# Performance work log

Hardware: AMD Instinct MI355X
Metric: run time of the kernel (lower is better)

## Reference

```python
import jax, jax.numpy as jnp
import numpy as np

B, N_IN, NODE, L = 4, 128, 32, 256
N_HID, N_OUT = 64, 128
D_IN = N_HID          # d_inner = expand(1) * d_model
D_STATE = 2 * N_HID   # d_state = n_hid * 2
D_CONV = 2
DT_RANK = max(1, -(-N_HID // 16))  # ceil(d_model/16) = 4


def setup_inputs() -> dict:
    key = jax.random.key(0)
    ks = jax.random.split(key, 12)
    s = lambda k, shape, scale: (jax.random.normal(k, shape, jnp.float32) * scale)
    inputs = jax.random.normal(ks[0], (B, N_IN, NODE, L), jnp.float32)
    return {
        "inputs": inputs,
        "w_in": s(ks[1], (N_HID, N_IN), 1.0 / np.sqrt(N_IN)),
        "b_in": jnp.zeros((N_HID,), jnp.float32),
        "in_proj_w": s(ks[2], (2 * D_IN, N_HID), 1.0 / np.sqrt(N_HID)),
        "conv_w": s(ks[3], (D_IN, D_CONV), 0.5),
        "conv_b": jnp.zeros((D_IN,), jnp.float32),
        "x_proj_w": s(ks[4], (DT_RANK + 2 * D_STATE, D_IN), 1.0 / np.sqrt(D_IN)),
        "dt_proj_w": s(ks[5], (D_IN, DT_RANK), DT_RANK ** -0.5),
        "dt_proj_b": s(ks[6], (D_IN,), 0.1),
        "A_log": jnp.log(jnp.tile(jnp.arange(1, D_STATE + 1, dtype=jnp.float32)[None, :], (D_IN, 1))),
        "D": jnp.ones((D_IN,), jnp.float32),
        "out_proj_w": s(ks[7], (N_HID, D_IN), 1.0 / np.sqrt(D_IN)),
        "w_out": s(ks[8], (N_OUT, N_HID), 1.0 / np.sqrt(N_HID)),
        "b_out": jnp.zeros((N_OUT,), jnp.float32),
        "ln_w": jnp.ones((L, N_OUT), jnp.float32),
        "ln_b": jnp.zeros((L, N_OUT), jnp.float32),
    }


def _mamba(x, in_proj_w, conv_w, conv_b, x_proj_w, dt_proj_w, dt_proj_b, A_log, D, out_proj_w):
    # x: (Bseq, L, d_model)
    Bs, Ls, _ = x.shape
    d_state = A_log.shape[1]
    dt_rank = dt_proj_w.shape[1]
    d_conv = conv_w.shape[1]

    xz = x @ in_proj_w.T                     # (Bs, L, 2*d_inner)
    xm, z = jnp.split(xz, 2, axis=-1)

    # causal depthwise conv1d (padding = d_conv-1, truncated to L)
    xp = jnp.pad(xm, ((0, 0), (d_conv - 1, 0), (0, 0)))
    xc = sum(xp[:, k:k + Ls, :] * conv_w[:, k] for k in range(d_conv)) + conv_b
    xc = jax.nn.silu(xc)                     # (Bs, L, d_inner)

    dbc = xc @ x_proj_w.T                    # (Bs, L, dt_rank + 2*d_state)
    dt = dbc[..., :dt_rank]
    Bm = dbc[..., dt_rank:dt_rank + d_state]
    Cm = dbc[..., dt_rank + d_state:]
    delta = jax.nn.softplus(dt @ dt_proj_w.T + dt_proj_b)  # (Bs, L, d_inner)
    A = -jnp.exp(A_log)                      # (d_inner, d_state)

    def step(h, inp):
        dlt, Bt, Ct, xt = inp                # (Bs,d), (Bs,s), (Bs,s), (Bs,d)
        dA = jnp.exp(dlt[:, :, None] * A)    # (Bs, d, s)
        h = dA * h + (dlt * xt)[:, :, None] * Bt[:, None, :]
        y = jnp.einsum('bds,bs->bd', h, Ct)
        return h, y

    h0 = jnp.zeros((Bs, xm.shape[-1], d_state), x.dtype)
    xs = (delta.transpose(1, 0, 2), Bm.transpose(1, 0, 2),
          Cm.transpose(1, 0, 2), xc.transpose(1, 0, 2))
    _, ys = jax.lax.scan(step, h0, xs)       # ys: (L, Bs, d_inner)

    y = ys.transpose(1, 0, 2) + xc * D
    y = y * jax.nn.silu(z)
    return y @ out_proj_w.T                  # (Bs, L, d_model)


def reference(inputs, w_in, b_in, in_proj_w, conv_w, conv_b, x_proj_w,
              dt_proj_w, dt_proj_b, A_log, D, out_proj_w,
              w_out, b_out, ln_w, ln_b):
    b, n_in, node, seq = inputs.shape
    # permute(0,2,3,1).reshape(B*node, L, n_in)
    x = inputs.transpose(0, 2, 3, 1).reshape(b * node, seq, n_in)
    x = x @ w_in.T + b_in
    x = jax.nn.silu(_mamba(x, in_proj_w, conv_w, conv_b, x_proj_w,
                           dt_proj_w, dt_proj_b, A_log, D, out_proj_w))
    x = x @ w_out.T + b_out                  # (B*node, L, n_out)
    # LayerNorm over last two dims [feature_len, n_out]
    mu = x.mean(axis=(-2, -1), keepdims=True)
    var = ((x - mu) ** 2).mean(axis=(-2, -1), keepdims=True)
    x = (x - mu) / jnp.sqrt(var + 1e-5) * ln_w + ln_b
    return x.reshape(b, node, seq, -1).transpose(0, 3, 1, 2)
```

## Files before the change

### kernel.cpp

```cpp
#include <hip/hip_runtime.h>
#include <math.h>


__device__ __forceinline__ float silu_f(float v) { return v / (1.f + __expf(-v)); }
__device__ __forceinline__ float softplus_f(float v) { return v > 20.f ? v : log1pf(__expf(v)); }

#if __has_builtin(__builtin_amdgcn_exp2f)
#define EXP2N(x) __builtin_amdgcn_exp2f(x)
#else
#define EXP2N(x) __expf((x) * 0.6931471805599453f)
#endif

__global__ __launch_bounds__(256) void k1_proj(
    const float* __restrict__ inp, const float* __restrict__ w_in,
    const float* __restrict__ b_in, const float* __restrict__ ipw,
    float* __restrict__ XM, float* __restrict__ Zb)
{
  __shared__ float sIN[128*64];
  __shared__ float sW[64*68];
  __shared__ float sXT[64*68];
  const int bid = blockIdx.x;
  const int r = bid >> 2, tb = bid & 3;
  const int b = r >> 5, node = r & 31;
  const int t0 = tb * 64;
  const int tid = threadIdx.x;
  const int tg = tid & 15, vg = tid >> 4;
  const int tl0 = tg * 4, v0 = vg * 4;

  for (int e = tid; e < 128*64; e += 256) {
    int i = e >> 6, t = e & 63;
    sIN[e] = inp[((b*128 + i)*32 + node)*256 + t0 + t];
  }

  float acc[4][4];
  #pragma unroll
  for (int ti = 0; ti < 4; ti++)
    #pragma unroll
    for (int j = 0; j < 4; j++) acc[ti][j] = b_in[v0 + j];

  for (int kc = 0; kc < 2; kc++) {
    __syncthreads();
    for (int e = tid; e < 64*16; e += 256) {
      int row = e >> 4, c4 = e & 15;
      *(float4*)&sW[row*68 + c4*4] = *(const float4*)&w_in[row*128 + kc*64 + c4*4];
    }
    __syncthreads();
    for (int k4 = 0; k4 < 16; k4++) {
      float4 wv[4];
      #pragma unroll
      for (int j = 0; j < 4; j++)
        wv[j] = *(const float4*)&sW[(v0 + j)*68 + k4*4];
      #pragma unroll
      for (int kk = 0; kk < 4; kk++) {
        float4 x4 = *(const float4*)&sIN[(kc*64 + k4*4 + kk)*64 + tl0];
        #pragma unroll
        for (int j = 0; j < 4; j++) {
          float w = kk==0 ? wv[j].x : kk==1 ? wv[j].y : kk==2 ? wv[j].z : wv[j].w;
          acc[0][j] = fmaf(x4.x, w, acc[0][j]);
          acc[1][j] = fmaf(x4.y, w, acc[1][j]);
          acc[2][j] = fmaf(x4.z, w, acc[2][j]);
          acc[3][j] = fmaf(x4.w, w, acc[3][j]);
        }
      }
    }
  }
  #pragma unroll
  for (int j = 0; j < 4; j++)
    *(float4*)&sXT[(v0 + j)*68 + tl0] =
        make_float4(acc[0][j], acc[1][j], acc[2][j], acc[3][j]);

  for (int pass = 0; pass < 2; pass++) {
    __syncthreads();
    for (int e = tid; e < 64*16; e += 256) {
      int row = e >> 4, c4 = e & 15;
      *(float4*)&sW[row*68 + c4*4] = *(const float4*)&ipw[(pass*64 + row)*64 + c4*4];
    }
    __syncthreads();

    float a2[4][4];
    #pragma unroll
    for (int ti = 0; ti < 4; ti++)
      #pragma unroll
      for (int j = 0; j < 4; j++) a2[ti][j] = 0.f;

    for (int k4 = 0; k4 < 16; k4++) {
      float4 wv[4];
      #pragma unroll
      for (int j = 0; j < 4; j++)
        wv[j] = *(const float4*)&sW[(v0 + j)*68 + k4*4];
      #pragma unroll
      for (int kk = 0; kk < 4; kk++) {
        float4 x4 = *(const float4*)&sXT[(k4*4 + kk)*68 + tl0];
        #pragma unroll
        for (int j = 0; j < 4; j++) {
          float w = kk==0 ? wv[j].x : kk==1 ? wv[j].y : kk==2 ? wv[j].z : wv[j].w;
          a2[0][j] = fmaf(x4.x, w, a2[0][j]);
          a2[1][j] = fmaf(x4.y, w, a2[1][j]);
          a2[2][j] = fmaf(x4.z, w, a2[2][j]);
          a2[3][j] = fmaf(x4.w, w, a2[3][j]);
        }
      }
    }

    float* dst = (pass == 0) ? XM : Zb;
    #pragma unroll
    for (int ti = 0; ti < 4; ti++)
      *(float4*)&dst[(r*256 + t0 + tl0 + ti)*64 + v0] =
          make_float4(a2[ti][0], a2[ti][1], a2[ti][2], a2[ti][3]);
  }
}

__global__ __launch_bounds__(256) void k2_conv_xproj(
    const float* __restrict__ XM, const float* __restrict__ convw,
    const float* __restrict__ convb, const float* __restrict__ xpw,
    const float* __restrict__ dtw, const float* __restrict__ dtb,
    float* __restrict__ XC, float* __restrict__ DELTA,
    float* __restrict__ BM, float* __restrict__ CM)
{
  __shared__ float sXM[65*64];
  __shared__ float sXC[64*68];
  __shared__ float sW[64*68];
  __shared__ float sDT[64*5];
  const int bid = blockIdx.x;
  const int r = bid >> 2, tb = bid & 3;
  const int t0 = tb * 64;
  const int tid = threadIdx.x;
  const int tg = tid & 15, vg = tid >> 4;
  const int tl0 = tg * 4, v0 = vg * 4;

  for (int e = tid; e < 65*64; e += 256) {
    int tt = e >> 6, d = e & 63;
    int tgl = t0 - 1 + tt;
    sXM[e] = (tgl < 0) ? 0.f : XM[(r*256 + tgl)*64 + d];
  }
  __syncthreads();

  for (int e = tid; e < 64*64; e += 256) {
    int t = e >> 6, d = e & 63;
    float c0 = convw[d*2], c1 = convw[d*2 + 1];
    float pre = fmaf(sXM[t*64 + d], c0, fmaf(sXM[(t+1)*64 + d], c1, convb[d]));
    float v = silu_f(pre);
    sXC[d*68 + t] = v;
    XC[(r*256 + t0 + t)*64 + d] = v;
  }

  for (int pass = 0; pass < 5; pass++) {
    __syncthreads();
    for (int e = tid; e < 64*16; e += 256) {
      int row = e >> 4, c4 = e & 15;
      int grow = pass*64 + row;
      float4 w = (grow < 260) ? *(const float4*)&xpw[grow*64 + c4*4]
                              : make_float4(0.f, 0.f, 0.f, 0.f);
      *(float4*)&sW[row*68 + c4*4] = w;
    }
    __syncthreads();

    float acc[4][4];
    #pragma unroll
    for (int ti = 0; ti < 4; ti++)
      #pragma unroll
      for (int jj = 0; jj < 4; jj++) acc[ti][jj] = 0.f;

    for (int k4 = 0; k4 < 16; k4++) {
      float4 wv[4];
      #pragma unroll
      for (int jj = 0; jj < 4; jj++)
        wv[jj] = *(const float4*)&sW[(v0 + jj)*68 + k4*4];
      #pragma unroll
      for (int kk = 0; kk < 4; kk++) {
        float4 x4 = *(const float4*)&sXC[(k4*4 + kk)*68 + tl0];
        #pragma unroll
        for (int jj = 0; jj < 4; jj++) {
          float w = kk==0 ? wv[jj].x : kk==1 ? wv[jj].y : kk==2 ? wv[jj].z : wv[jj].w;
          acc[0][jj] = fmaf(x4.x, w, acc[0][jj]);
          acc[1][jj] = fmaf(x4.y, w, acc[1][jj]);
          acc[2][jj] = fmaf(x4.z, w, acc[2][jj]);
          acc[3][jj] = fmaf(x4.w, w, acc[3][jj]);
        }
      }
    }

    const int j0g = pass*64 + v0;
    if (j0g < 4) {
      #pragma unroll
      for (int ti = 0; ti < 4; ti++)
        #pragma unroll
        for (int jj = 0; jj < 4; jj++)
          sDT[(tl0 + ti)*5 + jj] = acc[ti][jj];
    } else if (j0g < 132) {
      #pragma unroll
      for (int ti = 0; ti < 4; ti++)
        *(float4*)&BM[(r*256 + t0 + tl0 + ti)*128 + (j0g - 4)] =
            make_float4(acc[ti][0], acc[ti][1], acc[ti][2], acc[ti][3]);
    } else if (j0g < 260) {
      #pragma unroll
      for (int ti = 0; ti < 4; ti++)
        *(float4*)&CM[(r*256 + t0 + tl0 + ti)*128 + (j0g - 132)] =
            make_float4(acc[ti][0], acc[ti][1], acc[ti][2], acc[ti][3]);
    }
  }
  __syncthreads();

  for (int e = tid; e < 64*64; e += 256) {
    int t = e >> 6, d = e & 63;
    float4 w4 = *(const float4*)&dtw[d*4];
    float x = dtb[d];
    x = fmaf(sDT[t*5 + 0], w4.x, x);
    x = fmaf(sDT[t*5 + 1], w4.y, x);
    x = fmaf(sDT[t*5 + 2], w4.z, x);
    x = fmaf(sDT[t*5 + 3], w4.w, x);
    DELTA[(r*256 + t0 + t)*64 + d] = softplus_f(x);
  }
}

__global__ __launch_bounds__(256) void k3_scan(
    const float* __restrict__ DELTA, const float* __restrict__ XC,
    const float* __restrict__ BM, const float* __restrict__ CM,
    const float* __restrict__ alog, float* __restrict__ YP)
{
  const int bid = blockIdx.x;
  const int r = bid & 127;
  const int rest = bid >> 7;
  const int sc = rest & 1;
  const int dc = rest >> 1;
  const int tid = threadIdx.x;
  const int dg = tid >> 4;
  const int sg = tid & 15;
  const int sl0 = sg * 4;
  const int d = dc*16 + dg;
  const float LOG2E = 1.44269504f;

  float a2[4], h[4];
  #pragma unroll
  for (int j = 0; j < 4; j++) {
    a2[j] = -expf(alog[d*128 + sc*64 + sl0 + j]) * LOG2E;
    h[j] = 0.f;
  }

  const float* pB = BM    + r*256*128 + sc*64 + sl0;
  const float* pC = CM    + r*256*128 + sc*64 + sl0;
  const float* pD = DELTA + r*256*64  + d;
  const float* pX = XC    + r*256*64  + d;
  float*       pY = YP + ((size_t)(sc*128 + r))*256*64 + d;

  float4 vB0, vC0, vB1, vC1, vB2, vC2, vB3, vC3;
  float  vD0, vX0, vD1, vX1, vD2, vX2, vD3, vX3;

#define K3_LD(SET, T_) do { \
    vB##SET = *(const float4*)(pB + (T_)*128); \
    vC##SET = *(const float4*)(pC + (T_)*128); \
    vD##SET = pD[(T_)*64]; \
    vX##SET = pX[(T_)*64]; \
  } while (0)

#define K3_STEP(SET, T_) do { \
    float dl = vD##SET, xv = vX##SET; \
    float4 Bv = vB##SET, Cv = vC##SET; \
    float u = dl * xv; \
    float y; \
    float dA0 = EXP2N(dl * a2[0]); \
    h[0] = fmaf(dA0, h[0], u * Bv.x); \
    y = h[0] * Cv.x; \
    float dA1 = EXP2N(dl * a2[1]); \
    h[1] = fmaf(dA1, h[1], u * Bv.y); \
    y = fmaf(h[1], Cv.y, y); \
    float dA2 = EXP2N(dl * a2[2]); \
    h[2] = fmaf(dA2, h[2], u * Bv.z); \
    y = fmaf(h[2], Cv.z, y); \
    float dA3 = EXP2N(dl * a2[3]); \
    h[3] = fmaf(dA3, h[3], u * Bv.w); \
    y = fmaf(h[3], Cv.w, y); \
    int yi; \
    yi = __builtin_amdgcn_update_dpp(__float_as_int(y), __float_as_int(y), \
                                     0x121, 0xf, 0xf, false); \
    y += __int_as_float(yi); \
    yi = __builtin_amdgcn_update_dpp(__float_as_int(y), __float_as_int(y), \
                                     0x122, 0xf, 0xf, false); \
    y += __int_as_float(yi); \
    yi = __builtin_amdgcn_update_dpp(__float_as_int(y), __float_as_int(y), \
                                     0x124, 0xf, 0xf, false); \
    y += __int_as_float(yi); \
    yi = __builtin_amdgcn_update_dpp(__float_as_int(y), __float_as_int(y), \
                                     0x128, 0xf, 0xf, false); \
    y += __int_as_float(yi); \
    if (sg == 0) pY[(T_)*64] = y; \
  } while (0)

  K3_LD(0, 0); K3_LD(1, 1); K3_LD(2, 2); K3_LD(3, 3);

  for (int t = 0; t < 252; t += 4) {
    K3_STEP(0, t);     K3_LD(0, t + 4);
    K3_STEP(1, t + 1); K3_LD(1, t + 5);
    K3_STEP(2, t + 2); K3_LD(2, t + 6);
    K3_STEP(3, t + 3); K3_LD(3, t + 7);
  }
  K3_STEP(0, 252);
  K3_STEP(1, 253);
  K3_STEP(2, 254);
  K3_STEP(3, 255);

#undef K3_LD
#undef K3_STEP
}

__global__ __launch_bounds__(256) void k4_post(
    const float* __restrict__ YP, const float* __restrict__ XC,
    const float* __restrict__ Zb, const float* __restrict__ Dp,
    const float* __restrict__ opw, const float* __restrict__ wout,
    const float* __restrict__ bout, float* __restrict__ out,
    float* __restrict__ PSTAT)
{
  __shared__ float sY[64*68];
  __shared__ float sU[64*68];
  __shared__ float sW[64*68];
  __shared__ float sRs[256], sRq[256];
  const int bid = blockIdx.x;
  const int r = bid >> 2, tb = bid & 3;
  const int b = r >> 5, node = r & 31;
  const int t0 = tb * 64;
  const int tid = threadIdx.x;
  const int tg = tid & 15, vg = tid >> 4;
  const int tl0 = tg * 4, v0 = vg * 4;

  for (int e = tid; e < 64*64; e += 256) {
    int t = e >> 6, d = e & 63;
    int idx = (r*256 + t0 + t)*64 + d;
    float y = YP[idx] + YP[2097152 + idx];
    float y2 = fmaf(XC[idx], Dp[d], y);
    sY[d*68 + t] = y2 * silu_f(Zb[idx]);
  }

  __syncthreads();
  for (int e = tid; e < 64*16; e += 256) {
    int row = e >> 4, c4 = e & 15;
    *(float4*)&sW[row*68 + c4*4] = *(const float4*)&opw[row*64 + c4*4];
  }
  __syncthreads();

  {
    float acc[4][4];
    #pragma unroll
    for (int ti = 0; ti < 4; ti++)
      #pragma unroll
      for (int j = 0; j < 4; j++) acc[ti][j] = 0.f;
    for (int k4 = 0; k4 < 16; k4++) {
      float4 wv[4];
      #pragma unroll
      for (int j = 0; j < 4; j++)
        wv[j] = *(const float4*)&sW[(v0 + j)*68 + k4*4];
      #pragma unroll
      for (int kk = 0; kk < 4; kk++) {
        float4 x4 = *(const float4*)&sY[(k4*4 + kk)*68 + tl0];
        #pragma unroll
        for (int j = 0; j < 4; j++) {
          float w = kk==0 ? wv[j].x : kk==1 ? wv[j].y : kk==2 ? wv[j].z : wv[j].w;
          acc[0][j] = fmaf(x4.x, w, acc[0][j]);
          acc[1][j] = fmaf(x4.y, w, acc[1][j]);
          acc[2][j] = fmaf(x4.z, w, acc[2][j]);
          acc[3][j] = fmaf(x4.w, w, acc[3][j]);
        }
      }
    }
    #pragma unroll
    for (int j = 0; j < 4; j++)
      *(float4*)&sU[(v0 + j)*68 + tl0] =
          make_float4(silu_f(acc[0][j]), silu_f(acc[1][j]),
                      silu_f(acc[2][j]), silu_f(acc[3][j]));
  }

  float s = 0.f, q = 0.f;
  for (int pass = 0; pass < 2; pass++) {
    __syncthreads();
    for (int e = tid; e < 64*16; e += 256) {
      int row = e >> 4, c4 = e & 15;
      *(float4*)&sW[row*68 + c4*4] = *(const float4*)&wout[(pass*64 + row)*64 + c4*4];
    }
    __syncthreads();

    float a2[4][4];
    #pragma unroll
    for (int ti = 0; ti < 4; ti++)
      #pragma unroll
      for (int j = 0; j < 4; j++) a2[ti][j] = bout[pass*64 + v0 + j];

    for (int k4 = 0; k4 < 16; k4++) {
      float4 wv[4];
      #pragma unroll
      for (int j = 0; j < 4; j++)
        wv[j] = *(const float4*)&sW[(v0 + j)*68 + k4*4];
      #pragma unroll
      for (int kk = 0; kk < 4; kk++) {
        float4 x4 = *(const float4*)&sU[(k4*4 + kk)*68 + tl0];
        #pragma unroll
        for (int j = 0; j < 4; j++) {
          float w = kk==0 ? wv[j].x : kk==1 ? wv[j].y : kk==2 ? wv[j].z : wv[j].w;
          a2[0][j] = fmaf(x4.x, w, a2[0][j]);
          a2[1][j] = fmaf(x4.y, w, a2[1][j]);
          a2[2][j] = fmaf(x4.z, w, a2[2][j]);
          a2[3][j] = fmaf(x4.w, w, a2[3][j]);
        }
      }
    }

    #pragma unroll
    for (int ti = 0; ti < 4; ti++)
      #pragma unroll
      for (int j = 0; j < 4; j++) {
        float v = a2[ti][j];
        s += v;
        q = fmaf(v, v, q);
      }
    #pragma unroll
    for (int j = 0; j < 4; j++) {
      int o = pass*64 + v0 + j;
      *(float4*)&out[((b*128 + o)*32 + node)*256 + t0 + tl0] =
          make_float4(a2[0][j], a2[1][j], a2[2][j], a2[3][j]);
    }
  }

  sRs[tid] = s; sRq[tid] = q;
  __syncthreads();
  for (int st = 128; st > 0; st >>= 1) {
    if (tid < st) { sRs[tid] += sRs[tid + st]; sRq[tid] += sRq[tid + st]; }
    __syncthreads();
  }
  if (tid == 0) { PSTAT[bid*2] = sRs[0]; PSTAT[bid*2 + 1] = sRq[0]; }
}

__global__ __launch_bounds__(256) void k5_ln(
    const float* __restrict__ PSTAT, const float* __restrict__ lnw,
    const float* __restrict__ lnb, float* __restrict__ out)
{
  __shared__ float sLW[32*129], sLB[32*129];
  const int bid = blockIdx.x;
  const int r = bid >> 3, tb = bid & 7;
  const int b = r >> 5, node = r & 31;
  const int t0 = tb * 32;
  const int tid = threadIdx.x;

  float s = 0.f, q = 0.f;
  #pragma unroll
  for (int p = 0; p < 4; p++) {
    s += PSTAT[(r*4 + p)*2];
    q += PSTAT[(r*4 + p)*2 + 1];
  }
  const float mu = s * (1.f / 32768.f);
  const float var = q * (1.f / 32768.f) - mu * mu;
  const float rstd = rsqrtf(var + 1e-5f);

  for (int e = tid; e < 32*128; e += 256) {
    int t = e >> 7, o = e & 127;
    sLW[t*129 + o] = lnw[(t0 + t)*128 + o];
    sLB[t*129 + o] = lnb[(t0 + t)*128 + o];
  }
  __syncthreads();

  for (int n = 0; n < 16; n++) {
    int t = tid & 31;
    int o = (tid >> 5) + n*8;
    int idx = ((b*128 + o)*32 + node)*256 + t0 + t;
    float v = out[idx];
    out[idx] = fmaf((v - mu) * rstd, sLW[t*129 + o], sLB[t*129 + o]);
  }
}

extern "C" void kernel_launch(void* const* d_in, const int* in_sizes, int n_in,
                              void* d_out, int out_size, void* d_ws, size_t ws_size,
                              hipStream_t stream)
{
  (void)in_sizes; (void)n_in; (void)out_size; (void)ws_size;
  const float* inp   = (const float*)d_in[0];
  const float* w_in  = (const float*)d_in[1];
  const float* b_in  = (const float*)d_in[2];
  const float* ipw   = (const float*)d_in[3];
  const float* convw = (const float*)d_in[4];
  const float* convb = (const float*)d_in[5];
  const float* xpw   = (const float*)d_in[6];
  const float* dtw   = (const float*)d_in[7];
  const float* dtb   = (const float*)d_in[8];
  const float* alog  = (const float*)d_in[9];
  const float* Dp    = (const float*)d_in[10];
  const float* opw   = (const float*)d_in[11];
  const float* wout  = (const float*)d_in[12];
  const float* bout  = (const float*)d_in[13];
  const float* lnw   = (const float*)d_in[14];
  const float* lnb   = (const float*)d_in[15];

  float* ws = (float*)d_ws;
  float* XM    = ws + 0;
  float* Zb    = ws + 2097152;
  float* XC    = ws + 4194304;
  float* DELTA = ws + 6291456;
  float* BM    = ws + 8388608;
  float* CM    = ws + 12582912;
  float* YP    = ws + 16777216;
  float* PSTAT = ws + 20971520;
  float* out   = (float*)d_out;

  k1_proj<<<dim3(512), dim3(256), 0, stream>>>(inp, w_in, b_in, ipw, XM, Zb);
  k2_conv_xproj<<<dim3(512), dim3(256), 0, stream>>>(XM, convw, convb, xpw, dtw, dtb,
                                                     XC, DELTA, BM, CM);
  k3_scan<<<dim3(1024), dim3(256), 0, stream>>>(DELTA, XC, BM, CM, alog, YP);
  k4_post<<<dim3(512), dim3(256), 0, stream>>>(YP, XC, Zb, Dp, opw, wout, bout, out, PSTAT);
  k5_ln<<<dim3(1024), dim3(256), 0, stream>>>(PSTAT, lnw, lnb, out);
}
```

Measured before the change: 185.8 us.

## Store DELTA, XC, Z and Y channel-major so the scan reads contiguous time vectors

Switches the intermediate buffers DELTA, XC, Zb and YP from time-major (t, d) to channel-major (d, t) layout across all four kernels. In the scan kernel each channel's delta and x are now loaded as float4 over four consecutive timesteps, and the output y is written as one float4 per four steps instead of one strided scalar per step. The intent is to cut strided single-float global traffic in the latency-bound scan loop. In exchange, k1 and k2 now write transposed and less coalesced, and k2 gains an extra barrier and a separate store pass for XC.

Result: no change. 183.3 us (-1.3%).

```diff
diff --git a/kernel.cpp b/kernel.cpp
--- a/kernel.cpp
+++ b/kernel.cpp
@@ -102,11 +102,17 @@
       }
     }
 
-    float* dst = (pass == 0) ? XM : Zb;
-    #pragma unroll
-    for (int ti = 0; ti < 4; ti++)
-      *(float4*)&dst[(r*256 + t0 + tl0 + ti)*64 + v0] =
-          make_float4(a2[ti][0], a2[ti][1], a2[ti][2], a2[ti][3]);
+    if (pass == 0) {
+      #pragma unroll
+      for (int ti = 0; ti < 4; ti++)
+        *(float4*)&XM[(r*256 + t0 + tl0 + ti)*64 + v0] =
+            make_float4(a2[ti][0], a2[ti][1], a2[ti][2], a2[ti][3]);
+    } else {
+      #pragma unroll
+      for (int j = 0; j < 4; j++)
+        *(float4*)&Zb[(r*64 + v0 + j)*256 + t0 + tl0] =
+            make_float4(a2[0][j], a2[1][j], a2[2][j], a2[3][j]);
+    }
   }
 }
 
@@ -139,9 +145,13 @@
     int t = e >> 6, d = e & 63;
     float c0 = convw[d*2], c1 = convw[d*2 + 1];
     float pre = fmaf(sXM[t*64 + d], c0, fmaf(sXM[(t+1)*64 + d], c1, convb[d]));
-    float v = silu_f(pre);
-    sXC[d*68 + t] = v;
-    XC[(r*256 + t0 + t)*64 + d] = v;
+    sXC[d*68 + t] = silu_f(pre);
+  }
+  __syncthreads();
+
+  for (int e = tid; e < 64*64; e += 256) {
+    int d = e >> 6, t = e & 63;
+    XC[(r*64 + d)*256 + t0 + t] = sXC[d*68 + t];
   }
 
   for (int pass = 0; pass < 5; pass++) {
@@ -202,14 +212,14 @@
   __syncthreads();
 
   for (int e = tid; e < 64*64; e += 256) {
-    int t = e >> 6, d = e & 63;
+    int d = e >> 6, t = e & 63;
     float4 w4 = *(const float4*)&dtw[d*4];
     float x = dtb[d];
     x = fmaf(sDT[t*5 + 0], w4.x, x);
     x = fmaf(sDT[t*5 + 1], w4.y, x);
     x = fmaf(sDT[t*5 + 2], w4.z, x);
     x = fmaf(sDT[t*5 + 3], w4.w, x);
-    DELTA[(r*256 + t0 + t)*64 + d] = softplus_f(x);
+    DELTA[(r*64 + d)*256 + t0 + t] = softplus_f(x);
   }
 }
 
@@ -239,22 +249,19 @@
 
   const float* pB = BM    + r*256*128 + sc*64 + sl0;
   const float* pC = CM    + r*256*128 + sc*64 + sl0;
-  const float* pD = DELTA + r*256*64  + d;
-  const float* pX = XC    + r*256*64  + d;
-  float*       pY = YP + ((size_t)(sc*128 + r))*256*64 + d;
+  const float* pD = DELTA + ((size_t)(r*64 + d))*256;
+  const float* pX = XC    + ((size_t)(r*64 + d))*256;
+  float*       pY = YP + ((size_t)((sc*128 + r)*64 + d))*256;
 
   float4 vB0, vC0, vB1, vC1, vB2, vC2, vB3, vC3;
-  float  vD0, vX0, vD1, vX1, vD2, vX2, vD3, vX3;
-
-#define K3_LD(SET, T_) do { \
+
+#define K3_LDBC(SET, T_) do { \
     vB##SET = *(const float4*)(pB + (T_)*128); \
     vC##SET = *(const float4*)(pC + (T_)*128); \
-    vD##SET = pD[(T_)*64]; \
-    vX##SET = pX[(T_)*64]; \
   } while (0)
 
-#define K3_STEP(SET, T_) do { \
-    float dl = vD##SET, xv = vX##SET; \
+#define K3_STEP(SET, DL_, XV_, YOUT_) do { \
+    float dl = (DL_), xv = (XV_); \
     float4 Bv = vB##SET, Cv = vC##SET; \
     float u = dl * xv; \
     float y; \
@@ -283,23 +290,30 @@
     yi = __builtin_amdgcn_update_dpp(__float_as_int(y), __float_as_int(y), \
                                      0x128, 0xf, 0xf, false); \
     y += __int_as_float(yi); \
-    if (sg == 0) pY[(T_)*64] = y; \
+    (YOUT_) = y; \
   } while (0)
 
-  K3_LD(0, 0); K3_LD(1, 1); K3_LD(2, 2); K3_LD(3, 3);
-
-  for (int t = 0; t < 252; t += 4) {
-    K3_STEP(0, t);     K3_LD(0, t + 4);
-    K3_STEP(1, t + 1); K3_LD(1, t + 5);
-    K3_STEP(2, t + 2); K3_LD(2, t + 6);
-    K3_STEP(3, t + 3); K3_LD(3, t + 7);
-  }
-  K3_STEP(0, 252);
-  K3_STEP(1, 253);
-  K3_STEP(2, 254);
-  K3_STEP(3, 255);
-
-#undef K3_LD
+  float4 d4c = *(const float4*)(pD + 0);
+  float4 x4c = *(const float4*)(pX + 0);
+  K3_LDBC(0, 0); K3_LDBC(1, 1); K3_LDBC(2, 2); K3_LDBC(3, 3);
+
+  for (int t = 0; t < 256; t += 4) {
+    float4 d4n, x4n;
+    if (t < 252) {
+      d4n = *(const float4*)(pD + t + 4);
+      x4n = *(const float4*)(pX + t + 4);
+    }
+    float4 yv;
+    K3_STEP(0, d4c.x, x4c.x, yv.x); if (t < 252) K3_LDBC(0, t + 4);
+    K3_STEP(1, d4c.y, x4c.y, yv.y); if (t < 252) K3_LDBC(1, t + 5);
+    K3_STEP(2, d4c.z, x4c.z, yv.z); if (t < 252) K3_LDBC(2, t + 6);
+    K3_STEP(3, d4c.w, x4c.w, yv.w); if (t < 252) K3_LDBC(3, t + 7);
+    if (sg == 0)
+      *(float4*)(pY + t) = yv;
+    if (t < 252) { d4c = d4n; x4c = x4n; }
+  }
+
+#undef K3_LDBC
 #undef K3_STEP
 }
 
@@ -323,11 +337,11 @@
   const int tl0 = tg * 4, v0 = vg * 4;
 
   for (int e = tid; e < 64*64; e += 256) {
-    int t = e >> 6, d = e & 63;
-    int idx = (r*256 + t0 + t)*64 + d;
-    float y = YP[idx] + YP[2097152 + idx];
-    float y2 = fmaf(XC[idx], Dp[d], y);
-    sY[d*68 + t] = y2 * silu_f(Zb[idx]);
+    int d = e >> 6, t = e & 63;
+    int idxT = (r*64 + d)*256 + t0 + t;
+    float y = YP[idxT] + YP[2097152 + idxT];
+    float y2 = fmaf(XC[idxT], Dp[d], y);
+    sY[d*68 + t] = y2 * silu_f(Zb[idxT]);
   }
 
   __syncthreads();
```
